# Kernel optimization log

Measured on AMD Instinct MI355X. Metric: run time of the kernel, lower is better.

## Reference

```python
import jax, jax.numpy as jnp
import numpy as np


def setup_inputs() -> dict:
    key = jax.random.key(0)
    ks = jax.random.split(key, 6)
    B, C, H, W = 4, 512, 64, 64
    C8 = C // 8
    NS = H * W  # broadcasting in the original forces num_styles == H*W
    x = jax.random.normal(ks[0], (B, C, H, W), dtype=jnp.float32)
    Wq = jax.random.normal(ks[1], (C8, C), dtype=jnp.float32) * 0.02
    bq = jnp.zeros((C8,), jnp.float32)
    Wk = jax.random.normal(ks[2], (C8, C), dtype=jnp.float32) * 0.02
    bk = jnp.zeros((C8,), jnp.float32)
    Wv = jax.random.normal(ks[3], (C, C), dtype=jnp.float32) * 0.02
    bv = jnp.zeros((C,), jnp.float32)
    gamma = jnp.full((1,), 0.5, jnp.float32)  # nonzero so attention path contributes
    style_idx = jax.random.randint(ks[4], (B,), 0, NS)
    return {"x": x, "Wq": Wq, "bq": bq, "Wk": Wk, "bk": bk,
            "Wv": Wv, "bv": bv, "gamma": gamma,
            "style_idx": style_idx, "num_styles": NS}


def reference(x, Wq, bq, Wk, bk, Wv, bv, gamma, style_idx, num_styles):
    B, C, H, W = x.shape
    N = H * W
    xf = x.reshape(B, C, N)                                   # [B,C,N]
    # 1x1 convs == per-pixel linear projections
    q = jnp.einsum('oc,bcn->bno', Wq, xf) + bq                # [B,N,C8]
    k = jnp.einsum('oc,bcn->bon', Wk, xf) + bk[None, :, None]  # [B,C8,N]
    v = jnp.einsum('oc,bcn->bon', Wv, xf) + bv[None, :, None]  # [B,C,N]
    attn = jax.nn.softmax(jnp.einsum('bno,bom->bnm', q, k), axis=2)  # [B,N,N]
    # style mask: num_styles everywhere, except [b, 0, style_idx[b]] = 0
    # (torch scatter_ with index shape [B,1,1] only touches row 0)
    sw = jnp.full((B, N, num_styles), jnp.asarray(num_styles, x.dtype))
    sw = sw.at[jnp.arange(B), 0, style_idx].set(0.0)
    attn = attn * sw
    attended = jnp.einsum('bcn,bmn->bcm', v, attn).reshape(B, C, H, W)
    return gamma * attended + x
```

## Files before the change

kernel.cpp:

```cpp
#include <hip/hip_runtime.h>

#define B_DIM 4
#define C_DIM 512
#define N_DIM 4096
#define NS_F 4096.0f
#define LOG2E_F 1.4426950408889634f

typedef __attribute__((ext_vector_type(8))) short bf16x8;
typedef __attribute__((ext_vector_type(4))) float f32x4;

__device__ __forceinline__ unsigned short f2bf(float f) {
    union { float f; unsigned int u; } a; a.f = f;
    unsigned int u = a.u;
    return (unsigned short)((u + 0x7fffu + ((u >> 16) & 1u)) >> 16);
}
__device__ __forceinline__ float bf2f(unsigned short s) {
    union { unsigned int u; float f; } a; a.u = ((unsigned int)s) << 16;
    return a.f;
}

__global__ __launch_bounds__(256) void wconv_kernel(
    const float* __restrict__ Wq, const float* __restrict__ Wk,
    const float* __restrict__ Wv, unsigned short* __restrict__ Wb)
{
    const int gid = blockIdx.x * 256 + threadIdx.x;
    const int flat = gid * 4;
    const float* src;
    if (flat < 32768)      src = Wq + flat;
    else if (flat < 65536) src = Wk + (flat - 32768);
    else                   src = Wv + (flat - 65536);
    float4 v = *(const float4*)src;
    ushort4 r;
    r.x = f2bf(v.x); r.y = f2bf(v.y); r.z = f2bf(v.z); r.w = f2bf(v.w);
    *(ushort4*)(Wb + flat) = r;
}

__global__ __launch_bounds__(256) void xt_kernel(
    const float* __restrict__ x, unsigned short* __restrict__ xT)
{
    const int b  = blockIdx.z;
    const int c0 = blockIdx.y * 64;
    const int n0 = blockIdx.x * 64;
    __shared__ float T[64][65];
    const int t   = threadIdx.x;
    const int l16 = t & 15;
    const int cr  = t >> 4;

    #pragma unroll
    for (int j = 0; j < 4; ++j) {
        const int c = cr + j * 16;
        float4 v = *(const float4*)(x + ((size_t)(b * C_DIM + c0 + c)) * N_DIM + n0 + l16 * 4);
        T[l16 * 4 + 0][c] = v.x;
        T[l16 * 4 + 1][c] = v.y;
        T[l16 * 4 + 2][c] = v.z;
        T[l16 * 4 + 3][c] = v.w;
    }
    __syncthreads();
    #pragma unroll
    for (int j = 0; j < 2; ++j) {
        const int chunk = t + j * 256;
        const int n  = chunk >> 3;
        const int c8 = (chunk & 7) * 8;
        bf16x8 r;
        #pragma unroll
        for (int e = 0; e < 8; ++e) r[e] = (short)f2bf(T[n][c8 + e]);
        *(bf16x8*)(xT + ((size_t)b * N_DIM + n0 + n) * 512 + c0 + c8) = r;
    }
}

__global__ __launch_bounds__(256, 2) void proj_kernel(
    const unsigned short* __restrict__ xT, const unsigned short* __restrict__ Wb,
    const float* __restrict__ bq, const float* __restrict__ bk,
    const float* __restrict__ bv,
    unsigned short* __restrict__ qB, unsigned short* __restrict__ kB,
    unsigned short* __restrict__ vB)
{
    const int ot = blockIdx.x;
    const int n0 = blockIdx.y * 64;
    const int b  = blockIdx.z;
    const int tid  = threadIdx.x;
    const int w    = tid >> 6;
    const int lane = tid & 63;
    const int lql  = lane & 15;
    const int lk4  = lane >> 4;

    f32x4 acc[4];
    #pragma unroll
    for (int og = 0; og < 4; ++og) acc[og] = (f32x4){0.f, 0.f, 0.f, 0.f};

    if (ot < 2) {
        const unsigned short* Wp = Wb + ot * 32768;
        const unsigned short* xa = xT + ((size_t)b * N_DIM + n0 + w * 16 + lql) * 512 + lk4 * 8;
        #pragma unroll
        for (int h = 0; h < 2; ++h) {
            bf16x8 af[8];
            #pragma unroll
            for (int i = 0; i < 8; ++i)
                af[i] = *(const bf16x8*)(xa + (h * 8 + i) * 32);
            #pragma unroll
            for (int i = 0; i < 8; ++i) {
                #pragma unroll
                for (int og = 0; og < 4; ++og) {
                    bf16x8 wf = *(const bf16x8*)(Wp + (size_t)(og * 16 + lql) * 512 + (h * 8 + i) * 32 + lk4 * 8);
                    acc[og] = __builtin_amdgcn_mfma_f32_16x16x32_bf16(af[i], wf, acc[og], 0, 0, 0);
                }
            }
        }
        const float* bias = (ot == 0) ? bq : bk;
        #pragma unroll
        for (int og = 0; og < 4; ++og) {
            const float bb = bias[og * 16 + lql];
            #pragma unroll
            for (int r = 0; r < 4; ++r) {
                const int n = n0 + w * 16 + lk4 * 4 + r;
                if (ot == 0) {
                    qB[((size_t)b * N_DIM + n) * 64 + og * 16 + lql] =
                        f2bf((acc[og][r] + bb) * LOG2E_F);
                } else {
                    const int o = og * 16 + lql;
                    kB[((size_t)b * N_DIM + n) * 64 + (o ^ ((n & 7) << 3))] =
                        f2bf(acc[og][r] + bb);
                }
            }
        }
    } else {
        const int cb0 = (ot - 2) * 64;
        const unsigned short* wa = Wb + 65536 + (size_t)(cb0 + w * 16 + lql) * 512 + lk4 * 8;
        const unsigned short* xb = xT + (size_t)b * N_DIM * 512;
        #pragma unroll
        for (int h = 0; h < 2; ++h) {
            bf16x8 af[8];
            #pragma unroll
            for (int i = 0; i < 8; ++i)
                af[i] = *(const bf16x8*)(wa + (h * 8 + i) * 32);
            #pragma unroll
            for (int i = 0; i < 8; ++i) {
                #pragma unroll
                for (int og = 0; og < 4; ++og) {
                    bf16x8 xf = *(const bf16x8*)(xb + (size_t)(n0 + og * 16 + lql) * 512 + (h * 8 + i) * 32 + lk4 * 8);
                    acc[og] = __builtin_amdgcn_mfma_f32_16x16x32_bf16(af[i], xf, acc[og], 0, 0, 0);
                }
            }
        }
        #pragma unroll
        for (int r = 0; r < 4; ++r) {
            const int c = cb0 + w * 16 + lk4 * 4 + r;
            const float bb = bv[c];
            #pragma unroll
            for (int og = 0; og < 4; ++og) {
                vB[((size_t)(b * C_DIM + c)) * N_DIM + n0 + og * 16 + lql] =
                    f2bf(acc[og][r] + bb);
            }
        }
    }
}

__global__ __launch_bounds__(256, 4) void flash_kernel(
    const unsigned short* __restrict__ qB,
    const unsigned short* __restrict__ kB,
    const unsigned short* __restrict__ vB,
    const float* __restrict__ x,
    const float* __restrict__ gamma,
    float* __restrict__ stats,
    float* __restrict__ out)
{
    const int bid   = blockIdx.x;
    const int low3  = bid & 7;
    const int b     = low3 >> 1;
    const int c0bit = low3 & 1;
    const int high  = bid >> 3;
    const int mt    = high >> 1;
    const int ch    = ((high & 1) << 1) | c0bit;
    const int m0    = mt * 64;

    const int tid  = threadIdx.x;
    const int w    = tid >> 6;
    const int lane = tid & 63;
    const int lql  = lane & 15;
    const int lk4  = lane >> 4;
    const int swz  = (lql & 7) << 3;

    __shared__ __align__(16) unsigned short Kl[2][4096];
    __shared__ __align__(16) unsigned short Pl[64][72];
    __shared__ float scl[64];
    __shared__ float ll[64];
    __shared__ int   fl[4];

    const unsigned short* qrow = qB + ((size_t)b * N_DIM + m0 + w * 16 + lql) * 64 + lk4 * 8;
    const bf16x8 qf0 = *(const bf16x8*)(qrow);
    const bf16x8 qf1 = *(const bf16x8*)(qrow + 32);

    f32x4 acc[2][4];
    #pragma unroll
    for (int cg = 0; cg < 2; ++cg)
        #pragma unroll
        for (int qg = 0; qg < 4; ++qg)
            acc[cg][qg] = (f32x4){0.f, 0.f, 0.f, 0.f};

    float m_run = -3.0e38f;
    float l_run = 0.f;

    const unsigned short* kbb = kB + (size_t)b * N_DIM * 64;
    const unsigned short* vbb = vB + (size_t)b * C_DIM * N_DIM;
    const int cs = ch * 128 + w * 32;

    {
        bf16x8 a0 = *(const bf16x8*)(kbb + tid * 8);
        bf16x8 a1 = *(const bf16x8*)(kbb + 2048 + tid * 8);
        *(bf16x8*)(&Kl[0][tid * 8]) = a0;
        *(bf16x8*)(&Kl[0][2048 + tid * 8]) = a1;
    }
    __syncthreads();

    int buf = 0;
    for (int t = 0; t < 64; ++t) {
        const int tn_ = (t + 1) & 63;
        const bf16x8 kn0 = *(const bf16x8*)(kbb + (size_t)tn_ * 4096 + tid * 8);
        const bf16x8 kn1 = *(const bf16x8*)(kbb + (size_t)tn_ * 4096 + 2048 + tid * 8);

        f32x4 s[4];
        #pragma unroll
        for (int g = 0; g < 4; ++g) {
            const unsigned short* kr = &Kl[buf][(g * 16 + lql) * 64];
            bf16x8 ka0 = *(const bf16x8*)(kr + ((lk4 * 8) ^ swz));
            bf16x8 ka1 = *(const bf16x8*)(kr + ((lk4 * 8 + 32) ^ swz));
            f32x4 z = (f32x4){0.f, 0.f, 0.f, 0.f};
            z = __builtin_amdgcn_mfma_f32_16x16x32_bf16(ka0, qf0, z, 0, 0, 0);
            z = __builtin_amdgcn_mfma_f32_16x16x32_bf16(ka1, qf1, z, 0, 0, 0);
            s[g] = z;
        }

        float pmax = s[0][0];
        #pragma unroll
        for (int g = 0; g < 4; ++g)
            #pragma unroll
            for (int r = 0; r < 4; ++r)
                pmax = fmaxf(pmax, s[g][r]);
        pmax = fmaxf(pmax, __shfl_xor(pmax, 16));
        pmax = fmaxf(pmax, __shfl_xor(pmax, 32));

        const int wflag = __any(pmax > m_run + 8.f);
        float scv = 1.f;
        if (wflag) {
            const float nm = fmaxf(m_run, pmax);
            scv = exp2f(m_run - nm);
            m_run = nm;
        }
        float p[4][4];
        float ps = 0.f;
        #pragma unroll
        for (int g = 0; g < 4; ++g)
            #pragma unroll
            for (int r = 0; r < 4; ++r) {
                p[g][r] = exp2f(s[g][r] - m_run);
                ps += p[g][r];
            }
        ps += __shfl_xor(ps, 16);
        ps += __shfl_xor(ps, 32);
        l_run = l_run * scv + ps;

        if (lk4 == 0) scl[w * 16 + lql] = scv;
        if (lane == 0) fl[w] = wflag;

        {
            unsigned short* prow = &Pl[w * 16 + lql][0];
            #pragma unroll
            for (int g = 0; g < 4; ++g) {
                unsigned int lo, hi;
                asm("v_cvt_pk_bf16_f32 %0, %1, %2" : "=v"(lo) : "v"(p[g][0]), "v"(p[g][1]));
                asm("v_cvt_pk_bf16_f32 %0, %1, %2" : "=v"(hi) : "v"(p[g][2]), "v"(p[g][3]));
                *(uint2*)(prow + g * 16 + lk4 * 4) = make_uint2(lo, hi);
            }
        }
        __syncthreads();

        *(bf16x8*)(&Kl[buf ^ 1][tid * 8]) = kn0;
        *(bf16x8*)(&Kl[buf ^ 1][2048 + tid * 8]) = kn1;

        const int bflag = fl[0] | fl[1] | fl[2] | fl[3];
        if (bflag) {
            float sc4[4];
            #pragma unroll
            for (int qg = 0; qg < 4; ++qg) sc4[qg] = scl[qg * 16 + lql];
            #pragma unroll
            for (int cg = 0; cg < 2; ++cg)
                #pragma unroll
                for (int qg = 0; qg < 4; ++qg) {
                    acc[cg][qg][0] *= sc4[qg];
                    acc[cg][qg][1] *= sc4[qg];
                    acc[cg][qg][2] *= sc4[qg];
                    acc[cg][qg][3] *= sc4[qg];
                }
        }

        bf16x8 pf[4][2];
        #pragma unroll
        for (int qg = 0; qg < 4; ++qg) {
            const unsigned short* pr = &Pl[qg * 16 + lql][0];
            pf[qg][0] = *(const bf16x8*)(pr + lk4 * 8);
            pf[qg][1] = *(const bf16x8*)(pr + lk4 * 8 + 32);
        }

        const int n0 = t * 64;
        const unsigned short* vpb = vbb + (size_t)(cs + lql) * N_DIM + n0 + lk4 * 8;
        __builtin_amdgcn_s_setprio(1);
        #pragma unroll
        for (int cg = 0; cg < 2; ++cg) {
            const unsigned short* vp = vpb + (size_t)cg * 16 * N_DIM;
            bf16x8 va0 = *(const bf16x8*)(vp);
            bf16x8 va1 = *(const bf16x8*)(vp + 32);
            #pragma unroll
            for (int qg = 0; qg < 4; ++qg) {
                acc[cg][qg] = __builtin_amdgcn_mfma_f32_16x16x32_bf16(va0, pf[qg][0], acc[cg][qg], 0, 0, 0);
                acc[cg][qg] = __builtin_amdgcn_mfma_f32_16x16x32_bf16(va1, pf[qg][1], acc[cg][qg], 0, 0, 0);
            }
        }
        __builtin_amdgcn_s_setprio(0);
        __syncthreads();
        buf ^= 1;
    }

    if (mt == 0 && ch == 0 && tid == 0) {
        stats[b * 2 + 0] = m_run;
        stats[b * 2 + 1] = l_run;
    }

    if (lk4 == 0) ll[w * 16 + lql] = l_run;
    __syncthreads();

    const float gns = gamma[0] * NS_F;
    float inv4[4];
    #pragma unroll
    for (int qg = 0; qg < 4; ++qg) inv4[qg] = 1.f / ll[qg * 16 + lql];

    #pragma unroll
    for (int cg = 0; cg < 2; ++cg) {
        #pragma unroll
        for (int r = 0; r < 4; ++r) {
            const int c = cs + cg * 16 + lk4 * 4 + r;
            const size_t rowb = ((size_t)b * C_DIM + c) * N_DIM;
            #pragma unroll
            for (int qg = 0; qg < 4; ++qg) {
                const int mg = m0 + qg * 16 + lql;
                out[rowb + mg] = fmaf(gns * inv4[qg], acc[cg][qg][r], x[rowb + mg]);
            }
        }
    }
}

__global__ __launch_bounds__(512) void patch_kernel(
    const unsigned short* __restrict__ qB,
    const unsigned short* __restrict__ kB,
    const unsigned short* __restrict__ vB,
    const float* __restrict__ stats,
    const float* __restrict__ gamma,
    const int* __restrict__ sidx,
    float* __restrict__ out)
{
    const int b = blockIdx.x;
    const int c = threadIdx.x;
    __shared__ float q0s[64];
    if (c < 64) q0s[c] = bf2f(qB[(size_t)b * N_DIM * 64 + c]);
    __syncthreads();
    const int s  = sidx[b];
    const int m7 = s & 7;
    const unsigned short* kr = kB + ((size_t)b * N_DIM + s) * 64;
    float logit = 0.f;
    #pragma unroll
    for (int dj = 0; dj < 8; ++dj) {
        const int slot = dj ^ m7;
        bf16x8 kv = *(const bf16x8*)(kr + slot * 8);
        #pragma unroll
        for (int e = 0; e < 8; ++e)
            logit = fmaf(bf2f((unsigned short)kv[e]), q0s[dj * 8 + e], logit);
    }
    const float corr = NS_F * exp2f(logit - stats[b * 2]) / stats[b * 2 + 1];
    const float g = gamma[0];
    const float vcs = bf2f(vB[((size_t)b * C_DIM + c) * N_DIM + s]);
    out[((size_t)b * C_DIM + c) * N_DIM] -= g * corr * vcs;
}

extern "C" void kernel_launch(void* const* d_in, const int* in_sizes, int n_in,
                              void* d_out, int out_size, void* d_ws, size_t ws_size,
                              hipStream_t stream)
{
    const float* x     = (const float*)d_in[0];
    const float* Wq    = (const float*)d_in[1];
    const float* bq    = (const float*)d_in[2];
    const float* Wk    = (const float*)d_in[3];
    const float* bk    = (const float*)d_in[4];
    const float* Wv    = (const float*)d_in[5];
    const float* bv    = (const float*)d_in[6];
    const float* gamma = (const float*)d_in[7];
    const int*   sidx  = (const int*)d_in[8];
    float* out = (float*)d_out;

    unsigned short* xT = (unsigned short*)d_ws;
    unsigned short* Wb = xT + (size_t)B_DIM * N_DIM * 512;
    unsigned short* qB = Wb + 327680;
    unsigned short* kB = qB + (size_t)B_DIM * N_DIM * 64;
    unsigned short* vB = kB + (size_t)B_DIM * N_DIM * 64;
    float* stats = (float*)(vB + (size_t)B_DIM * C_DIM * N_DIM);

    wconv_kernel<<<dim3(320), 256, 0, stream>>>(Wq, Wk, Wv, Wb);
    xt_kernel<<<dim3(64, 8, B_DIM), 256, 0, stream>>>(x, xT);
    proj_kernel<<<dim3(10, 64, B_DIM), 256, 0, stream>>>(xT, Wb, bq, bk, bv, qB, kB, vB);
    flash_kernel<<<dim3(1024), 256, 0, stream>>>(qB, kB, vB, x, gamma, stats, out);
    patch_kernel<<<dim3(B_DIM), 512, 0, stream>>>(qB, kB, vB, stats, gamma, sidx, out);
}
```

Measured before the change: 366.7 us.

## Fuse projection tiles into one block with shared-memory x tile; swizzle P buffer

The projection kernel now loads each 64-pixel x tile into LDS once, using an XOR swizzle, and computes all Q, K and V output tiles from it. Before, ten separate blocks each reread the same x rows from global memory. This cuts the grid from 2560 blocks to 256 and uses 64KB of LDS per block, which lowers parallelism and occupancy for the projection stage. Separately, the flash kernel's P buffer drops its row padding in favour of an XOR-swizzled layout, and the inline-asm packed bf16 conversion is replaced with software rounding, which adds ALU work.

```diff
diff --git a/kernel.cpp b/kernel.cpp
--- a/kernel.cpp
+++ b/kernel.cpp
@@ -68,42 +68,52 @@
     }
 }
 
-__global__ __launch_bounds__(256, 2) void proj_kernel(
+__global__ __launch_bounds__(256) void projf_kernel(
     const unsigned short* __restrict__ xT, const unsigned short* __restrict__ Wb,
     const float* __restrict__ bq, const float* __restrict__ bk,
     const float* __restrict__ bv,
     unsigned short* __restrict__ qB, unsigned short* __restrict__ kB,
     unsigned short* __restrict__ vB)
 {
-    const int ot = blockIdx.x;
-    const int n0 = blockIdx.y * 64;
-    const int b  = blockIdx.z;
+    const int n0 = blockIdx.x * 64;
+    const int b  = blockIdx.y;
     const int tid  = threadIdx.x;
     const int w    = tid >> 6;
     const int lane = tid & 63;
     const int lql  = lane & 15;
     const int lk4  = lane >> 4;
-
-    f32x4 acc[4];
-    #pragma unroll
-    for (int og = 0; og < 4; ++og) acc[og] = (f32x4){0.f, 0.f, 0.f, 0.f};
-
-    if (ot < 2) {
+    const int l7   = lql & 7;
+
+    __shared__ __align__(16) unsigned short xs[64][512];
+
+    {
+        const unsigned short* xTb = xT + (size_t)b * N_DIM * 512;
+        #pragma unroll
+        for (int j = 0; j < 16; ++j) {
+            const int chunk = tid + j * 256;
+            const int n  = chunk >> 6;
+            const int c8 = chunk & 63;
+            bf16x8 v = *(const bf16x8*)(xTb + (size_t)(n0 + n) * 512 + c8 * 8);
+            *(bf16x8*)(&xs[n][((c8 ^ (n & 7)) * 8)]) = v;
+        }
+    }
+    __syncthreads();
+
+    #pragma unroll
+    for (int ot = 0; ot < 2; ++ot) {
         const unsigned short* Wp = Wb + ot * 32768;
-        const unsigned short* xa = xT + ((size_t)b * N_DIM + n0 + w * 16 + lql) * 512 + lk4 * 8;
-        #pragma unroll
-        for (int h = 0; h < 2; ++h) {
-            bf16x8 af[8];
-            #pragma unroll
-            for (int i = 0; i < 8; ++i)
-                af[i] = *(const bf16x8*)(xa + (h * 8 + i) * 32);
-            #pragma unroll
-            for (int i = 0; i < 8; ++i) {
-                #pragma unroll
-                for (int og = 0; og < 4; ++og) {
-                    bf16x8 wf = *(const bf16x8*)(Wp + (size_t)(og * 16 + lql) * 512 + (h * 8 + i) * 32 + lk4 * 8);
-                    acc[og] = __builtin_amdgcn_mfma_f32_16x16x32_bf16(af[i], wf, acc[og], 0, 0, 0);
-                }
+        const int arow = w * 16 + lql;
+        const int a7 = arow & 7;
+        f32x4 acc[4];
+        #pragma unroll
+        for (int og = 0; og < 4; ++og) acc[og] = (f32x4){0.f, 0.f, 0.f, 0.f};
+        #pragma unroll
+        for (int ks = 0; ks < 16; ++ks) {
+            bf16x8 a = *(const bf16x8*)(&xs[arow][((ks * 4 + lk4) ^ a7) * 8]);
+            #pragma unroll
+            for (int og = 0; og < 4; ++og) {
+                bf16x8 wf = *(const bf16x8*)(Wp + (size_t)(og * 16 + lql) * 512 + ks * 32 + lk4 * 8);
+                acc[og] = __builtin_amdgcn_mfma_f32_16x16x32_bf16(a, wf, acc[og], 0, 0, 0);
             }
         }
         const float* bias = (ot == 0) ? bq : bk;
@@ -123,23 +133,23 @@
                 }
             }
         }
-    } else {
-        const int cb0 = (ot - 2) * 64;
+    }
+
+    #pragma unroll
+    for (int vt = 0; vt < 8; ++vt) {
+        const int cb0 = vt * 64;
         const unsigned short* wa = Wb + 65536 + (size_t)(cb0 + w * 16 + lql) * 512 + lk4 * 8;
-        const unsigned short* xb = xT + (size_t)b * N_DIM * 512;
-        #pragma unroll
-        for (int h = 0; h < 2; ++h) {
-            bf16x8 af[8];
-            #pragma unroll
-            for (int i = 0; i < 8; ++i)
-                af[i] = *(const bf16x8*)(wa + (h * 8 + i) * 32);
-            #pragma unroll
-            for (int i = 0; i < 8; ++i) {
-                #pragma unroll
-                for (int og = 0; og < 4; ++og) {
-                    bf16x8 xf = *(const bf16x8*)(xb + (size_t)(n0 + og * 16 + lql) * 512 + (h * 8 + i) * 32 + lk4 * 8);
-                    acc[og] = __builtin_amdgcn_mfma_f32_16x16x32_bf16(af[i], xf, acc[og], 0, 0, 0);
-                }
+        f32x4 acc[4];
+        #pragma unroll
+        for (int og = 0; og < 4; ++og) acc[og] = (f32x4){0.f, 0.f, 0.f, 0.f};
+        #pragma unroll
+        for (int ks = 0; ks < 16; ++ks) {
+            bf16x8 a = *(const bf16x8*)(wa + ks * 32);
+            #pragma unroll
+            for (int og = 0; og < 4; ++og) {
+                const int brow = og * 16 + lql;
+                bf16x8 xf = *(const bf16x8*)(&xs[brow][((ks * 4 + lk4) ^ l7) * 8]);
+                acc[og] = __builtin_amdgcn_mfma_f32_16x16x32_bf16(a, xf, acc[og], 0, 0, 0);
             }
         }
         #pragma unroll
@@ -181,7 +191,7 @@
     const int swz  = (lql & 7) << 3;
 
     __shared__ __align__(16) unsigned short Kl[2][4096];
-    __shared__ __align__(16) unsigned short Pl[64][72];
+    __shared__ __align__(16) unsigned short Pl[4096];
     __shared__ float scl[64];
     __shared__ float ll[64];
     __shared__ int   fl[4];
@@ -263,13 +273,12 @@
         if (lane == 0) fl[w] = wflag;
 
         {
-            unsigned short* prow = &Pl[w * 16 + lql][0];
+            const int prow = (w * 16 + lql) * 64;
             #pragma unroll
             for (int g = 0; g < 4; ++g) {
-                unsigned int lo, hi;
-                asm("v_cvt_pk_bf16_f32 %0, %1, %2" : "=v"(lo) : "v"(p[g][0]), "v"(p[g][1]));
-                asm("v_cvt_pk_bf16_f32 %0, %1, %2" : "=v"(hi) : "v"(p[g][2]), "v"(p[g][3]));
-                *(uint2*)(prow + g * 16 + lk4 * 4) = make_uint2(lo, hi);
+                unsigned int lo = (unsigned int)f2bf(p[g][0]) | ((unsigned int)f2bf(p[g][1]) << 16);
+                unsigned int hi = (unsigned int)f2bf(p[g][2]) | ((unsigned int)f2bf(p[g][3]) << 16);
+                *(uint2*)(&Pl[prow + ((g * 16 + lk4 * 4) ^ swz)]) = make_uint2(lo, hi);
             }
         }
         __syncthreads();
@@ -296,9 +305,9 @@
         bf16x8 pf[4][2];
         #pragma unroll
         for (int qg = 0; qg < 4; ++qg) {
-            const unsigned short* pr = &Pl[qg * 16 + lql][0];
-            pf[qg][0] = *(const bf16x8*)(pr + lk4 * 8);
-            pf[qg][1] = *(const bf16x8*)(pr + lk4 * 8 + 32);
+            const unsigned short* pr = &Pl[(qg * 16 + lql) * 64];
+            pf[qg][0] = *(const bf16x8*)(pr + ((lk4 * 8) ^ swz));
+            pf[qg][1] = *(const bf16x8*)(pr + ((lk4 * 8 + 32) ^ swz));
         }
 
         const int n0 = t * 64;
@@ -404,7 +413,7 @@
 
     wconv_kernel<<<dim3(320), 256, 0, stream>>>(Wq, Wk, Wv, Wb);
     xt_kernel<<<dim3(64, 8, B_DIM), 256, 0, stream>>>(x, xT);
-    proj_kernel<<<dim3(10, 64, B_DIM), 256, 0, stream>>>(xT, Wb, bq, bk, bv, qB, kB, vB);
+    projf_kernel<<<dim3(64, B_DIM), 256, 0, stream>>>(xT, Wb, bq, bk, bv, qB, kB, vB);
     flash_kernel<<<dim3(1024), 256, 0, stream>>>(qB, kB, vB, x, gamma, stats, out);
     patch_kernel<<<dim3(B_DIM), 512, 0, stream>>>(qB, kB, vB, stats, gamma, sidx, out);
 }
```

Measured after the change: 316.1 us. -13.8%, faster.
